# Kernel tuning notes

Hardware: AMD Instinct MI355X
Metric: run time of the kernel (lower is better)

The kernel has to match this reference:

```python
import jax, jax.numpy as jnp
import numpy as np

EMB = 512
HEADS = 8

def setup_inputs() -> dict:
    key = jax.random.key(0)
    ks = jax.random.split(key, 9)
    s = 1.0 / np.sqrt(EMB)
    return {
        'x':  jax.random.normal(ks[0], (4, 2048, EMB), dtype=jnp.float32),
        'Wq': jax.random.uniform(ks[1], (EMB, EMB), jnp.float32, -s, s),
        'bq': jax.random.uniform(ks[2], (EMB,), jnp.float32, -s, s),
        'Wk': jax.random.uniform(ks[3], (EMB, EMB), jnp.float32, -s, s),
        'bk': jax.random.uniform(ks[4], (EMB,), jnp.float32, -s, s),
        'Wv': jax.random.uniform(ks[5], (EMB, EMB), jnp.float32, -s, s),
        'bv': jax.random.uniform(ks[6], (EMB,), jnp.float32, -s, s),
        'Wo': jax.random.uniform(ks[7], (EMB, EMB), jnp.float32, -s, s),
        'bo': jax.random.uniform(ks[8], (EMB,), jnp.float32, -s, s),
    }

def reference(x, Wq, bq, Wk, bk, Wv, bv, Wo, bo):
    b, n, e = x.shape
    h = HEADS
    d = e // h
    def split_heads(t):
        return t.reshape(b, n, h, d).transpose(0, 2, 1, 3)  # b h n d
    q = split_heads(x @ Wq.T + bq)
    k = split_heads(x @ Wk.T + bk)
    v = split_heads(x @ Wv.T + bv)
    energy = jnp.einsum('bhqd,bhkd->bhqk', q, k)
    scaling = jnp.sqrt(jnp.float32(e))  # NOTE: sqrt(emb_size), not sqrt(head_dim), per source
    att = jax.nn.softmax(energy / scaling, axis=-1)
    out = jnp.einsum('bhal,bhlv->bhav', att, v)  # b h n d
    out = out.transpose(0, 2, 1, 3).reshape(b, n, e)
    return out @ Wo.T + bo
```

## Files before the change

kernel.cpp:

```cpp
#include <hip/hip_runtime.h>

typedef float f32x4 __attribute__((ext_vector_type(4)));
typedef float f32x16 __attribute__((ext_vector_type(16)));
typedef short bf16x8 __attribute__((ext_vector_type(8)));
typedef unsigned int uint;
typedef unsigned short ushort_t;

#define EMB    512
#define NSEQ   2048
#define NBATCH 4
#define NHEAD  8
#define MROWS  (NBATCH * NSEQ)
#define CEXP   0.06375872f

__device__ __forceinline__ uint f2bf(float x) {
    uint u = __builtin_bit_cast(uint, x);
    return (u + 0x7fffu + ((u >> 16) & 1u)) >> 16;
}

__device__ __forceinline__ void glds16(const void* g, void* l) {
    __builtin_amdgcn_global_load_lds(
        (const __attribute__((address_space(1))) uint*)g,
        (__attribute__((address_space(3))) uint*)l, 16, 0, 0);
}

__global__ __launch_bounds__(256)
void prep(const float* __restrict__ x,
          const float* __restrict__ Wq, const float* __restrict__ Wk,
          const float* __restrict__ Wv, const float* __restrict__ Wo,
          const float* __restrict__ bq, const float* __restrict__ bk,
          const float* __restrict__ bv,
          ushort_t* __restrict__ xb, ushort_t* __restrict__ Wqkvb,
          float* __restrict__ bqkv, ushort_t* __restrict__ Wob) {
    int t = blockIdx.x * 256 + threadIdx.x;
    {
        float4 v = ((const float4*)x)[t];
        uint2 p;
        p.x = f2bf(v.x) | (f2bf(v.y) << 16);
        p.y = f2bf(v.z) | (f2bf(v.w) << 16);
        ((uint2*)xb)[t] = p;
    }
    if (t < 65536) {
        float4 a = ((const float4*)Wq)[t];
        float4 b = ((const float4*)Wk)[t];
        float4 c = ((const float4*)Wv)[t];
        float4 d = ((const float4*)Wo)[t];
        uint2 p;
        p.x = f2bf(a.x) | (f2bf(a.y) << 16); p.y = f2bf(a.z) | (f2bf(a.w) << 16);
        ((uint2*)Wqkvb)[t] = p;
        p.x = f2bf(b.x) | (f2bf(b.y) << 16); p.y = f2bf(b.z) | (f2bf(b.w) << 16);
        ((uint2*)Wqkvb)[t + 65536] = p;
        p.x = f2bf(c.x) | (f2bf(c.y) << 16); p.y = f2bf(c.z) | (f2bf(c.w) << 16);
        ((uint2*)Wqkvb)[t + 131072] = p;
        p.x = f2bf(d.x) | (f2bf(d.y) << 16); p.y = f2bf(d.z) | (f2bf(d.w) << 16);
        ((uint2*)Wob)[t] = p;
    }
    if (t < 512) {
        bqkv[t] = bq[t]; bqkv[512 + t] = bk[t]; bqkv[1024 + t] = bv[t];
    }
}

template<int MODE>
__global__ __launch_bounds__(256)
void gemm128(const ushort_t* __restrict__ A, const ushort_t* __restrict__ BT,
             const float* __restrict__ bias, ushort_t* __restrict__ oQK,
             ushort_t* __restrict__ oVT, float* __restrict__ oC) {
    __shared__ ushort_t As[128][32];
    __shared__ ushort_t Bs[128][32];
    __shared__ float ep[32][132];
    const int tid = threadIdx.x, wave = tid >> 6, lane = tid & 63;
    const int m0 = blockIdx.x * 128, n0 = blockIdx.y * 128;
    const int wr = (wave & 1) * 64, wc = (wave >> 1) * 64;

    f32x4 acc[4][4];
#pragma unroll
    for (int i = 0; i < 4; ++i)
#pragma unroll
        for (int j = 0; j < 4; ++j) acc[i][j] = (f32x4){0.f, 0.f, 0.f, 0.f};

    const int grow = wave * 16 + (lane >> 2);
    const int gcol = (lane & 3) * 8;
    const ushort_t* Ag = A  + (size_t)(m0 + grow) * 512 + gcol;
    const ushort_t* Bg = BT + (size_t)(n0 + grow) * 512 + gcol;
    ushort_t* lA0 = &As[wave * 16][0];
    ushort_t* lA1 = &As[64 + wave * 16][0];
    ushort_t* lB0 = &Bs[wave * 16][0];
    ushort_t* lB1 = &Bs[64 + wave * 16][0];
    const int fr = lane & 15, fc = (lane >> 4) * 8;

    for (int kt = 0; kt < 16; ++kt) {
        __syncthreads();
        glds16(Ag + kt * 32,             lA0);
        glds16(Ag + kt * 32 + 64 * 512,  lA1);
        glds16(Bg + kt * 32,             lB0);
        glds16(Bg + kt * 32 + 64 * 512,  lB1);
        __syncthreads();
        bf16x8 af[4], bf[4];
#pragma unroll
        for (int i = 0; i < 4; ++i) af[i] = *(const bf16x8*)&As[wr + i * 16 + fr][fc];
#pragma unroll
        for (int j = 0; j < 4; ++j) bf[j] = *(const bf16x8*)&Bs[wc + j * 16 + fr][fc];
#pragma unroll
        for (int i = 0; i < 4; ++i)
#pragma unroll
            for (int j = 0; j < 4; ++j)
                acc[i][j] = __builtin_amdgcn_mfma_f32_16x16x32_bf16(af[i], bf[j], acc[i][j], 0, 0, 0);
    }

    const int col_l = lane & 15, row_l = (lane >> 4) * 4;

    if (MODE == 0 && n0 >= 1024) {
#pragma unroll
        for (int j = 0; j < 4; ++j) {
            const int col = n0 + wc + j * 16 + col_l;
            const float bv = bias[col];
#pragma unroll
            for (int i = 0; i < 4; ++i) {
                const int row = m0 + wr + i * 16 + row_l;
                f32x4 v = acc[i][j];
                v += (f32x4){bv, bv, bv, bv};
                const int e = col - 1024;
                const int b = row >> 11, tok = row & 2047;
                uint2 p;
                p.x = f2bf(v[0]) | (f2bf(v[1]) << 16);
                p.y = f2bf(v[2]) | (f2bf(v[3]) << 16);
                *(uint2*)&oVT[((size_t)(b * 512 + e)) * 2048 + tok] = p;
            }
        }
        return;
    }

    const float scale = (MODE == 0 && n0 < 512) ? CEXP : 1.0f;
    float bv[4];
#pragma unroll
    for (int j = 0; j < 4; ++j) bv[j] = bias[n0 + wc + j * 16 + col_l];

    const int erow = tid >> 3, eseg = (tid & 7) * 16;
#pragma unroll
    for (int c = 0; c < 4; ++c) {
        __syncthreads();
        if (wr == (c >> 1) * 64) {
#pragma unroll
            for (int ii = 0; ii < 2; ++ii) {
                const int i = (c & 1) * 2 + ii;
#pragma unroll
                for (int j = 0; j < 4; ++j) {
                    f32x4 v = acc[i][j];
#pragma unroll
                    for (int r = 0; r < 4; ++r)
                        ep[ii * 16 + row_l + r][wc + j * 16 + col_l] = (v[r] + bv[j]) * scale;
                }
            }
        }
        __syncthreads();
        const int grow2 = m0 + c * 32 + erow;
        if (MODE == 0) {
            uint4 o0, o1;
#pragma unroll
            for (int k = 0; k < 4; ++k) {
                uint lo = f2bf(ep[erow][eseg + k * 2])     | (f2bf(ep[erow][eseg + k * 2 + 1]) << 16);
                uint hi = f2bf(ep[erow][eseg + 8 + k * 2]) | (f2bf(ep[erow][eseg + 9 + k * 2]) << 16);
                ((uint*)&o0)[k] = lo; ((uint*)&o1)[k] = hi;
            }
            *(uint4*)&oQK[(size_t)grow2 * 1024 + n0 + eseg]     = o0;
            *(uint4*)&oQK[(size_t)grow2 * 1024 + n0 + eseg + 8] = o1;
        } else {
#pragma unroll
            for (int k = 0; k < 4; ++k) {
                f32x4 v = *(const f32x4*)&ep[erow][eseg + k * 4];
                *(f32x4*)&oC[(size_t)grow2 * 512 + n0 + eseg + k * 4] = v;
            }
        }
    }
}

template<int NSLICE>
__global__ __launch_bounds__(256, 4)
void attn_mfma(const ushort_t* __restrict__ QK, const ushort_t* __restrict__ VT,
               ushort_t* __restrict__ Op, float* __restrict__ Lp,
               ushort_t* __restrict__ AO) {
    __shared__ ushort_t Ks[64][72];
    __shared__ ushort_t Vs[64][72];

    const int tid = threadIdx.x, w = tid >> 6, lane = tid & 63;
    const int qt = blockIdx.x, bh = blockIdx.y, b = bh >> 3, h = bh & 7;
    const int slice = (NSLICE > 1) ? blockIdx.z : 0;
    const int l31 = lane & 31, lhi = lane >> 5;

    const int tok = qt * 128 + w * 32 + l31;
    const size_t qrow = (size_t)(b * NSEQ + tok);
    bf16x8 qf[4];
#pragma unroll
    for (int ks = 0; ks < 4; ++ks)
        qf[ks] = *(const bf16x8*)&QK[qrow * 1024 + h * 64 + ks * 16 + lhi * 8];

    f32x16 accO[2];
#pragma unroll
    for (int i = 0; i < 16; ++i) { accO[0][i] = 0.f; accO[1][i] = 0.f; }
    float lpart = 0.f;

    const int sr = tid & 63, sc = (tid >> 6) * 16;
    const ushort_t* Kg = QK + (size_t)(b * NSEQ) * 1024 + 512 + h * 64;
    const ushort_t* Vg = VT + ((size_t)(b * 512 + h * 64)) * 2048;

    const int kt0 = slice * (32 / NSLICE), kt1 = kt0 + 32 / NSLICE;
    for (int kt = kt0; kt < kt1; ++kt) {
        const int k0 = kt * 64;
        uint4 kv0 = *(const uint4*)&Kg[(size_t)(k0 + sr) * 1024 + sc];
        uint4 kv1 = *(const uint4*)&Kg[(size_t)(k0 + sr) * 1024 + sc + 8];
        uint4 vv0 = *(const uint4*)&Vg[(size_t)sr * 2048 + k0 + sc];
        uint4 vv1 = *(const uint4*)&Vg[(size_t)sr * 2048 + k0 + sc + 8];
        __syncthreads();
        *(uint4*)&Ks[sr][sc] = kv0;  *(uint4*)&Ks[sr][sc + 8] = kv1;
        *(uint4*)&Vs[sr][sc] = vv0;  *(uint4*)&Vs[sr][sc + 8] = vv1;
        __syncthreads();

#pragma unroll
        for (int ms = 0; ms < 2; ++ms) {
            f32x16 st;
#pragma unroll
            for (int i = 0; i < 16; ++i) st[i] = 0.f;
#pragma unroll
            for (int ks = 0; ks < 4; ++ks) {
                bf16x8 ka = *(const bf16x8*)&Ks[ms * 32 + l31][ks * 16 + lhi * 8];
                st = __builtin_amdgcn_mfma_f32_32x32x16_bf16(ka, qf[ks], st, 0, 0, 0);
            }
            uint dd[8], ee[8];
#pragma unroll
            for (int i = 0; i < 8; ++i) {
                uint ua = __builtin_bit_cast(uint, __builtin_amdgcn_exp2f(st[2 * i]));
                uint ub = __builtin_bit_cast(uint, __builtin_amdgcn_exp2f(st[2 * i + 1]));
                lpart += __builtin_bit_cast(float, ua & 0xffff0000u)
                       + __builtin_bit_cast(float, ub & 0xffff0000u);
                dd[i] = (ua >> 16) | (ub & 0xffff0000u);
            }
#pragma unroll
            for (int i = 0; i < 8; ++i) ee[i] = (uint)__shfl_xor((int)dd[i], 32);
#pragma unroll
            for (int s = 0; s < 2; ++s) {
                union { uint u[4]; bf16x8 v; } B;
                B.u[0] = lhi ? ee[4 * s + 2] : dd[4 * s + 0];
                B.u[1] = lhi ? ee[4 * s + 3] : dd[4 * s + 1];
                B.u[2] = lhi ? dd[4 * s + 2] : ee[4 * s + 0];
                B.u[3] = lhi ? dd[4 * s + 3] : ee[4 * s + 1];
                const int step = ms * 2 + s;
                bf16x8 va0 = *(const bf16x8*)&Vs[l31][step * 16 + lhi * 8];
                bf16x8 va1 = *(const bf16x8*)&Vs[32 + l31][step * 16 + lhi * 8];
                accO[0] = __builtin_amdgcn_mfma_f32_32x32x16_bf16(va0, B.v, accO[0], 0, 0, 0);
                accO[1] = __builtin_amdgcn_mfma_f32_32x32x16_bf16(va1, B.v, accO[1], 0, 0, 0);
            }
        }
    }

    const float lfull = lpart + __shfl_xor(lpart, 32);

    if (NSLICE == 1) {
        const float inv = 1.0f / lfull;
#pragma unroll
        for (int hf = 0; hf < 2; ++hf)
#pragma unroll
            for (int r = 0; r < 16; ++r) {
                const int d = (r & 3) + 8 * (r >> 2) + 4 * lhi + 32 * hf;
                AO[((size_t)(b * NSEQ + tok)) * 512 + h * 64 + d] =
                    (ushort_t)f2bf(accO[hf][r] * inv);
            }
    } else {
        if (lane < 32) Lp[(size_t)slice * 65536 + bh * 2048 + tok] = lfull;
        ushort_t* Os = Op + (size_t)slice * 4194304;
#pragma unroll
        for (int hf = 0; hf < 2; ++hf)
#pragma unroll
            for (int r = 0; r < 16; ++r) {
                const int d = (r & 3) + 8 * (r >> 2) + 4 * lhi + 32 * hf;
                Os[((size_t)(bh * 64 + d)) * 2048 + tok] = (ushort_t)f2bf(accO[hf][r]);
            }
    }
}

__global__ __launch_bounds__(256)
void combine4T(const ushort_t* __restrict__ Op, const float* __restrict__ Lp,
               ushort_t* __restrict__ AO) {
    __shared__ float T[64][68];
    const int tid = threadIdx.x;
    const int tc = blockIdx.x, bh = blockIdx.y;
    const int b = bh >> 3, h = bh & 7;
    const int tok0 = tc * 64;

    const int d = tid >> 2, ts = (tid & 3) * 16;
    float acc[16];
#pragma unroll
    for (int i = 0; i < 16; ++i) acc[i] = 0.f;
#pragma unroll
    for (int s = 0; s < 4; ++s) {
        const ushort_t* P = Op + (size_t)s * 4194304
                               + ((size_t)(bh * 64 + d)) * 2048 + tok0 + ts;
#pragma unroll
        for (int k2 = 0; k2 < 2; ++k2) {
            uint4 u = *(const uint4*)(P + 8 * k2);
#pragma unroll
            for (int j = 0; j < 4; ++j) {
                uint uw = ((const uint*)&u)[j];
                acc[k2 * 8 + 2 * j]     += __builtin_bit_cast(float, uw << 16);
                acc[k2 * 8 + 2 * j + 1] += __builtin_bit_cast(float, uw & 0xffff0000u);
            }
        }
    }
#pragma unroll
    for (int k = 0; k < 4; ++k)
        *(f32x4*)&T[d][ts + 4 * k] = *(const f32x4*)&acc[4 * k];
    __syncthreads();

    const int tk = tid >> 2, ds = (tid & 3) * 16;
    const int tok = tok0 + tk;
    const float l = Lp[bh * 2048 + tok]           + Lp[65536 + bh * 2048 + tok]
                  + Lp[131072 + bh * 2048 + tok]  + Lp[196608 + bh * 2048 + tok];
    const float inv = 1.0f / l;
    uint o[8];
#pragma unroll
    for (int k = 0; k < 8; ++k) {
        float a = T[ds + 2 * k][tk] * inv;
        float c = T[ds + 2 * k + 1][tk] * inv;
        o[k] = f2bf(a) | (f2bf(c) << 16);
    }
    ushort_t* dst = AO + ((size_t)(b * NSEQ + tok)) * 512 + h * 64 + ds;
    *(uint4*)dst       = *(const uint4*)&o[0];
    *(uint4*)(dst + 8) = *(const uint4*)&o[4];
}

extern "C" void kernel_launch(void* const* d_in, const int* in_sizes, int n_in,
                              void* d_out, int out_size, void* d_ws, size_t ws_size,
                              hipStream_t stream) {
    const float* x  = (const float*)d_in[0];
    const float* Wq = (const float*)d_in[1];
    const float* bq = (const float*)d_in[2];
    const float* Wk = (const float*)d_in[3];
    const float* bk = (const float*)d_in[4];
    const float* Wv = (const float*)d_in[5];
    const float* bv = (const float*)d_in[6];
    const float* Wo = (const float*)d_in[7];
    const float* bo = (const float*)d_in[8];

    char* ws = (char*)d_ws;
    ushort_t* xb    = (ushort_t*)(ws);
    ushort_t* Wqkvb = (ushort_t*)(ws + 8388608);
    ushort_t* Wob   = (ushort_t*)(ws + 9961472);
    float*    bqkv  = (float*)   (ws + 10485760);
    ushort_t* QKb   = (ushort_t*)(ws + 10491904);
    ushort_t* VTg   = (ushort_t*)(ws + 27269120);
    ushort_t* AOb   = (ushort_t*)(ws + 35657728);
    ushort_t* Opart = (ushort_t*)(ws + 44046336);
    float*    Lpart = (float*)   (ws);
    const bool split = ws_size >= 78125056;

    prep<<<4096, 256, 0, stream>>>(x, Wq, Wk, Wv, Wo, bq, bk, bv,
                                   xb, Wqkvb, bqkv, Wob);
    gemm128<0><<<dim3(64, 12), 256, 0, stream>>>(xb, Wqkvb, bqkv, QKb, VTg, nullptr);
    if (split) {
        attn_mfma<4><<<dim3(16, 32, 4), 256, 0, stream>>>(QKb, VTg, Opart, Lpart, nullptr);
        combine4T<<<dim3(32, 32), 256, 0, stream>>>(Opart, Lpart, AOb);
    } else {
        attn_mfma<1><<<dim3(16, 32, 1), 256, 0, stream>>>(QKb, VTg, nullptr, nullptr, AOb);
    }
    gemm128<1><<<dim3(64, 4), 256, 0, stream>>>(AOb, Wob, bo, nullptr, nullptr, (float*)d_out);
}
```

Baseline: 187.5 us.

## Process two query groups per wave in attention and halve the KV split count

Each wave now handles 64 query tokens (two 32-row groups), so every K/V tile staged in LDS feeds twice as many MFMAs and the K fragments are loaded once for both groups. The grid shrinks to 8 query tiles per head, the key-split factor drops from 4 to 2, and the combine kernel sums only two partials, which cuts partial-output traffic. In exchange register pressure rises, so launch bounds drop to 3 blocks per CU. Fewer blocks may also reduce latency hiding.

```diff
diff --git a/kernel.cpp b/kernel.cpp
--- a/kernel.cpp
+++ b/kernel.cpp
@@ -175,7 +175,7 @@
 }
 
 template<int NSLICE>
-__global__ __launch_bounds__(256, 4)
+__global__ __launch_bounds__(256, 3)
 void attn_mfma(const ushort_t* __restrict__ QK, const ushort_t* __restrict__ VT,
                ushort_t* __restrict__ Op, float* __restrict__ Lp,
                ushort_t* __restrict__ AO) {
@@ -187,17 +187,21 @@
     const int slice = (NSLICE > 1) ? blockIdx.z : 0;
     const int l31 = lane & 31, lhi = lane >> 5;
 
-    const int tok = qt * 128 + w * 32 + l31;
-    const size_t qrow = (size_t)(b * NSEQ + tok);
-    bf16x8 qf[4];
-#pragma unroll
-    for (int ks = 0; ks < 4; ++ks)
-        qf[ks] = *(const bf16x8*)&QK[qrow * 1024 + h * 64 + ks * 16 + lhi * 8];
-
-    f32x16 accO[2];
-#pragma unroll
-    for (int i = 0; i < 16; ++i) { accO[0][i] = 0.f; accO[1][i] = 0.f; }
-    float lpart = 0.f;
+    const int tok0 = qt * 256 + w * 64 + l31;
+    bf16x8 qf[2][4];
+#pragma unroll
+    for (int g = 0; g < 2; ++g)
+#pragma unroll
+        for (int ks = 0; ks < 4; ++ks)
+            qf[g][ks] = *(const bf16x8*)&QK[(size_t)(b * NSEQ + tok0 + g * 32) * 1024
+                                            + h * 64 + ks * 16 + lhi * 8];
+
+    f32x16 accO[2][2];
+#pragma unroll
+    for (int g = 0; g < 2; ++g)
+#pragma unroll
+        for (int i = 0; i < 16; ++i) { accO[g][0][i] = 0.f; accO[g][1][i] = 0.f; }
+    float lpart[2] = {0.f, 0.f};
 
     const int sr = tid & 63, sc = (tid >> 6) * 16;
     const ushort_t* Kg = QK + (size_t)(b * NSEQ) * 1024 + 512 + h * 64;
@@ -217,69 +221,98 @@
 
 #pragma unroll
         for (int ms = 0; ms < 2; ++ms) {
-            f32x16 st;
-#pragma unroll
-            for (int i = 0; i < 16; ++i) st[i] = 0.f;
+            bf16x8 ka[4];
+#pragma unroll
+            for (int ks = 0; ks < 4; ++ks)
+                ka[ks] = *(const bf16x8*)&Ks[ms * 32 + l31][ks * 16 + lhi * 8];
+
+            f32x16 st[2];
+#pragma unroll
+            for (int g = 0; g < 2; ++g)
+#pragma unroll
+                for (int i = 0; i < 16; ++i) st[g][i] = 0.f;
 #pragma unroll
             for (int ks = 0; ks < 4; ++ks) {
-                bf16x8 ka = *(const bf16x8*)&Ks[ms * 32 + l31][ks * 16 + lhi * 8];
-                st = __builtin_amdgcn_mfma_f32_32x32x16_bf16(ka, qf[ks], st, 0, 0, 0);
-            }
-            uint dd[8], ee[8];
-#pragma unroll
-            for (int i = 0; i < 8; ++i) {
-                uint ua = __builtin_bit_cast(uint, __builtin_amdgcn_exp2f(st[2 * i]));
-                uint ub = __builtin_bit_cast(uint, __builtin_amdgcn_exp2f(st[2 * i + 1]));
-                lpart += __builtin_bit_cast(float, ua & 0xffff0000u)
-                       + __builtin_bit_cast(float, ub & 0xffff0000u);
-                dd[i] = (ua >> 16) | (ub & 0xffff0000u);
-            }
-#pragma unroll
-            for (int i = 0; i < 8; ++i) ee[i] = (uint)__shfl_xor((int)dd[i], 32);
+                st[0] = __builtin_amdgcn_mfma_f32_32x32x16_bf16(ka[ks], qf[0][ks], st[0], 0, 0, 0);
+                st[1] = __builtin_amdgcn_mfma_f32_32x32x16_bf16(ka[ks], qf[1][ks], st[1], 0, 0, 0);
+            }
+
+            uint dd[2][8], ee[2][8];
+#pragma unroll
+            for (int g = 0; g < 2; ++g)
+#pragma unroll
+                for (int i = 0; i < 8; ++i) {
+                    uint ua = __builtin_bit_cast(uint, __builtin_amdgcn_exp2f(st[g][2 * i]));
+                    uint ub = __builtin_bit_cast(uint, __builtin_amdgcn_exp2f(st[g][2 * i + 1]));
+                    lpart[g] += __builtin_bit_cast(float, ua & 0xffff0000u)
+                              + __builtin_bit_cast(float, ub & 0xffff0000u);
+                    dd[g][i] = (ua >> 16) | (ub & 0xffff0000u);
+                }
+#pragma unroll
+            for (int g = 0; g < 2; ++g)
+#pragma unroll
+                for (int i = 0; i < 8; ++i)
+                    ee[g][i] = (uint)__shfl_xor((int)dd[g][i], 32);
+
 #pragma unroll
             for (int s = 0; s < 2; ++s) {
-                union { uint u[4]; bf16x8 v; } B;
-                B.u[0] = lhi ? ee[4 * s + 2] : dd[4 * s + 0];
-                B.u[1] = lhi ? ee[4 * s + 3] : dd[4 * s + 1];
-                B.u[2] = lhi ? dd[4 * s + 2] : ee[4 * s + 0];
-                B.u[3] = lhi ? dd[4 * s + 3] : ee[4 * s + 1];
                 const int step = ms * 2 + s;
                 bf16x8 va0 = *(const bf16x8*)&Vs[l31][step * 16 + lhi * 8];
                 bf16x8 va1 = *(const bf16x8*)&Vs[32 + l31][step * 16 + lhi * 8];
-                accO[0] = __builtin_amdgcn_mfma_f32_32x32x16_bf16(va0, B.v, accO[0], 0, 0, 0);
-                accO[1] = __builtin_amdgcn_mfma_f32_32x32x16_bf16(va1, B.v, accO[1], 0, 0, 0);
-            }
-        }
-    }
-
-    const float lfull = lpart + __shfl_xor(lpart, 32);
+#pragma unroll
+                for (int g = 0; g < 2; ++g) {
+                    union { uint u[4]; bf16x8 v; } B;
+                    B.u[0] = lhi ? ee[g][4 * s + 2] : dd[g][4 * s + 0];
+                    B.u[1] = lhi ? ee[g][4 * s + 3] : dd[g][4 * s + 1];
+                    B.u[2] = lhi ? dd[g][4 * s + 2] : ee[g][4 * s + 0];
+                    B.u[3] = lhi ? dd[g][4 * s + 3] : ee[g][4 * s + 1];
+                    accO[g][0] = __builtin_amdgcn_mfma_f32_32x32x16_bf16(va0, B.v, accO[g][0], 0, 0, 0);
+                    accO[g][1] = __builtin_amdgcn_mfma_f32_32x32x16_bf16(va1, B.v, accO[g][1], 0, 0, 0);
+                }
+            }
+        }
+    }
+
+    float lfull[2];
+#pragma unroll
+    for (int g = 0; g < 2; ++g) lfull[g] = lpart[g] + __shfl_xor(lpart[g], 32);
 
     if (NSLICE == 1) {
-        const float inv = 1.0f / lfull;
-#pragma unroll
-        for (int hf = 0; hf < 2; ++hf)
-#pragma unroll
-            for (int r = 0; r < 16; ++r) {
-                const int d = (r & 3) + 8 * (r >> 2) + 4 * lhi + 32 * hf;
-                AO[((size_t)(b * NSEQ + tok)) * 512 + h * 64 + d] =
-                    (ushort_t)f2bf(accO[hf][r] * inv);
-            }
+#pragma unroll
+        for (int g = 0; g < 2; ++g) {
+            const float inv = 1.0f / lfull[g];
+#pragma unroll
+            for (int hf = 0; hf < 2; ++hf)
+#pragma unroll
+                for (int r = 0; r < 16; ++r) {
+                    const int d = (r & 3) + 8 * (r >> 2) + 4 * lhi + 32 * hf;
+                    AO[((size_t)(b * NSEQ + tok0 + g * 32)) * 512 + h * 64 + d] =
+                        (ushort_t)f2bf(accO[g][hf][r] * inv);
+                }
+        }
     } else {
-        if (lane < 32) Lp[(size_t)slice * 65536 + bh * 2048 + tok] = lfull;
+        if (lane < 32) {
+#pragma unroll
+            for (int g = 0; g < 2; ++g)
+                Lp[(size_t)slice * 65536 + bh * 2048 + tok0 + g * 32] = lfull[g];
+        }
         ushort_t* Os = Op + (size_t)slice * 4194304;
 #pragma unroll
-        for (int hf = 0; hf < 2; ++hf)
-#pragma unroll
-            for (int r = 0; r < 16; ++r) {
-                const int d = (r & 3) + 8 * (r >> 2) + 4 * lhi + 32 * hf;
-                Os[((size_t)(bh * 64 + d)) * 2048 + tok] = (ushort_t)f2bf(accO[hf][r]);
-            }
+        for (int g = 0; g < 2; ++g)
+#pragma unroll
+            for (int hf = 0; hf < 2; ++hf)
+#pragma unroll
+                for (int r = 0; r < 16; ++r) {
+                    const int d = (r & 3) + 8 * (r >> 2) + 4 * lhi + 32 * hf;
+                    Os[((size_t)(bh * 64 + d)) * 2048 + tok0 + g * 32] =
+                        (ushort_t)f2bf(accO[g][hf][r]);
+                }
     }
 }
 
 __global__ __launch_bounds__(256)
-void combine4T(const ushort_t* __restrict__ Op, const float* __restrict__ Lp,
-               ushort_t* __restrict__ AO) {
+void combine2Tb(const ushort_t* __restrict__ Op, const float* __restrict__ Lp,
+                ushort_t* __restrict__ AO) {
     __shared__ float T[64][68];
     const int tid = threadIdx.x;
     const int tc = blockIdx.x, bh = blockIdx.y;
@@ -291,7 +324,7 @@
 #pragma unroll
     for (int i = 0; i < 16; ++i) acc[i] = 0.f;
 #pragma unroll
-    for (int s = 0; s < 4; ++s) {
+    for (int s = 0; s < 2; ++s) {
         const ushort_t* P = Op + (size_t)s * 4194304
                                + ((size_t)(bh * 64 + d)) * 2048 + tok0 + ts;
 #pragma unroll
@@ -312,9 +345,7 @@
 
     const int tk = tid >> 2, ds = (tid & 3) * 16;
     const int tok = tok0 + tk;
-    const float l = Lp[bh * 2048 + tok]           + Lp[65536 + bh * 2048 + tok]
-                  + Lp[131072 + bh * 2048 + tok]  + Lp[196608 + bh * 2048 + tok];
-    const float inv = 1.0f / l;
+    const float inv = 1.0f / (Lp[bh * 2048 + tok] + Lp[65536 + bh * 2048 + tok]);
     uint o[8];
 #pragma unroll
     for (int k = 0; k < 8; ++k) {
@@ -356,10 +387,10 @@
                                    xb, Wqkvb, bqkv, Wob);
     gemm128<0><<<dim3(64, 12), 256, 0, stream>>>(xb, Wqkvb, bqkv, QKb, VTg, nullptr);
     if (split) {
-        attn_mfma<4><<<dim3(16, 32, 4), 256, 0, stream>>>(QKb, VTg, Opart, Lpart, nullptr);
-        combine4T<<<dim3(32, 32), 256, 0, stream>>>(Opart, Lpart, AOb);
+        attn_mfma<2><<<dim3(8, 32, 2), 256, 0, stream>>>(QKb, VTg, Opart, Lpart, nullptr);
+        combine2Tb<<<dim3(32, 32), 256, 0, stream>>>(Opart, Lpart, AOb);
     } else {
-        attn_mfma<1><<<dim3(16, 32, 1), 256, 0, stream>>>(QKb, VTg, nullptr, nullptr, AOb);
+        attn_mfma<1><<<dim3(8, 32, 1), 256, 0, stream>>>(QKb, VTg, nullptr, nullptr, AOb);
     }
     gemm128<1><<<dim3(64, 4), 256, 0, stream>>>(AOb, Wob, bo, nullptr, nullptr, (float*)d_out);
 }
```

Result: faster. 183.3 us (-2.3%).
